# Performance work log

Hardware: AMD Instinct MI355X
Metric: run time of the kernel (lower is better)

Reference implementation:

```python
import jax, jax.numpy as jnp
import numpy as np

B, T, E, H = 8, 1024, 1024, 16
D = E // H  # head_dim = 64
MAX_OFFSET = 0.5


def setup_inputs() -> dict:
    key = jax.random.key(0)
    ks = jax.random.split(key, 12)
    s = 0.02
    return {
        "query": jax.random.normal(ks[0], (B, T, E), jnp.float32),
        "key_": jax.random.normal(ks[1], (B, T, E), jnp.float32),
        "value": jax.random.normal(ks[2], (B, T, E), jnp.float32),
        "Wq": jax.random.normal(ks[3], (E, E), jnp.float32) * s,
        "bq": jnp.zeros((E,), jnp.float32),
        "Wk": jax.random.normal(ks[4], (E, E), jnp.float32) * s,
        "bk": jnp.zeros((E,), jnp.float32),
        "Wv": jax.random.normal(ks[5], (E, E), jnp.float32) * s,
        "bv": jnp.zeros((E,), jnp.float32),
        "Wo": jax.random.normal(ks[6], (E, E), jnp.float32) * s,
        "bo": jnp.zeros((E,), jnp.float32),
        "bias_table": jax.random.normal(ks[7], (2 * T - 1, H), jnp.float32) * s,
        "offset": jax.random.normal(ks[8], (1,), jnp.float32) * 0.1,
    }


def _temporal_bias(bias_table, offset):
    # relative position index: [T, T] in [0, 2T-2]
    coords = jnp.arange(T)
    rel = (coords[:, None] - coords[None, :]) + (T - 1)
    bounded = jnp.tanh(offset) * MAX_OFFSET  # scalar (shape (1,))
    adj = jnp.clip(rel.astype(jnp.float32) + bounded, 0.0, 2.0 * T - 2.0)
    lo = jnp.floor(adj).astype(jnp.int32)
    hi = jnp.ceil(adj).astype(jnp.int32)
    w = adj - lo.astype(jnp.float32)  # [T, T]
    lo_val = bias_table[lo]  # [T, T, H]
    hi_val = bias_table[hi]  # [T, T, H]
    bias = lo_val * (1.0 - w[..., None]) + hi_val * w[..., None]
    # -> [1, H, T, T]
    return jnp.transpose(bias, (2, 0, 1))[None]


def reference(query, key_, value, Wq, bq, Wk, bk, Wv, bv, Wo, bo, bias_table, offset):
    scale = D ** -0.5
    # torch Linear: x @ W.T + b
    q = (jnp.einsum('bte,fe->btf', query, Wq) + bq).reshape(B, T, H, D).transpose(0, 2, 1, 3)
    k = (jnp.einsum('bte,fe->btf', key_, Wk) + bk).reshape(B, T, H, D).transpose(0, 2, 1, 3)
    v = (jnp.einsum('bte,fe->btf', value, Wv) + bv).reshape(B, T, H, D).transpose(0, 2, 1, 3)
    scores = jnp.einsum('bhqd,bhkd->bhqk', q, k) * scale  # [B, H, T, T]
    scores = scores + _temporal_bias(bias_table, offset)
    attn = jax.nn.softmax(scores, axis=-1)
    out = jnp.einsum('bhqk,bhkd->bhqd', attn, v)  # [B, H, T, D]
    out = out.transpose(0, 2, 1, 3).reshape(B, T, E)
    return jnp.einsum('bte,fe->btf', out, Wo) + bo
```

## Files before the change

### kernel.cpp

```cpp
#include <hip/hip_runtime.h>
#include <hip/hip_bf16.h>
#include <stdint.h>

#define B_ 8
#define T_ 1024
#define E_ 1024
#define H_ 16
#define D_ 64
#define NREL 2047

using bf16 = __hip_bfloat16;
typedef __attribute__((ext_vector_type(8))) short bhalf8;
typedef __attribute__((ext_vector_type(4))) float f32x4;

typedef __attribute__((address_space(3))) uint32_t lds32_t;
typedef const __attribute__((address_space(1))) uint32_t glb32_t;
__device__ __forceinline__ void gld_lds16(const bf16* g, bf16* l) {
  __builtin_amdgcn_global_load_lds((glb32_t*)(const void*)g, (lds32_t*)(void*)l, 16, 0, 0);
}

__device__ __forceinline__ bhalf8 cvt8(const float4 a, const float4 b) {
  bf16 t[8];
  t[0] = __float2bfloat16(a.x); t[1] = __float2bfloat16(a.y);
  t[2] = __float2bfloat16(a.z); t[3] = __float2bfloat16(a.w);
  t[4] = __float2bfloat16(b.x); t[5] = __float2bfloat16(b.y);
  t[6] = __float2bfloat16(b.z); t[7] = __float2bfloat16(b.w);
  return *(const bhalf8*)t;
}

__global__ __launch_bounds__(256) void cvt_w4b(const float* __restrict__ Wq,
                                               const float* __restrict__ Wk,
                                               const float* __restrict__ Wv,
                                               const float* __restrict__ Wo,
                                               bf16* __restrict__ d,
                                               const float* __restrict__ table,
                                               const float* __restrict__ offset,
                                               float* __restrict__ db) {
  const int z = blockIdx.y;
  if (z == 4) {
    const int idx = blockIdx.x * 256 + threadIdx.x;
    if (idx >= NREL * H_) return;
    const int r = idx >> 4;
    const int h = idx & 15;
    const float bounded = tanhf(offset[0]) * 0.5f;
    float adj = (float)r + bounded;
    adj = fminf(fmaxf(adj, 0.f), 2046.f);
    const int lo = (int)floorf(adj);
    const int hi = (int)ceilf(adj);
    const float wgt = adj - (float)lo;
    const float v = table[lo * H_ + h] * (1.f - wgt) + table[hi * H_ + h] * wgt;
    db[h * NREL + r] = v * 1.4426950408889634f;
    return;
  }
  const float* s = (z == 0) ? Wq : (z == 1) ? Wk : (z == 2) ? Wv : Wo;
  const int i = (blockIdx.x * 256 + threadIdx.x) * 8;
  const float4 a = *(const float4*)(s + i);
  const float4 b = *(const float4*)(s + i + 4);
  *(bhalf8*)(d + (size_t)z * E_ * E_ + i) = cvt8(a, b);
}

__global__ __launch_bounds__(256, 3) void gemm_qkv(const float* __restrict__ Xq,
                                                   const float* __restrict__ Xk,
                                                   const float* __restrict__ Xv,
                                                   const bf16* __restrict__ Wc,
                                                   const float* __restrict__ bqp,
                                                   const float* __restrict__ bkp,
                                                   const float* __restrict__ bvp,
                                                   bf16* __restrict__ dst) {
  __shared__ bf16 As[2 * 128 * 32];
  __shared__ bf16 Bs[3 * 128 * 32];
  const int tid = threadIdx.x;
  const int lane = tid & 63;
  const int w = tid >> 6;
  const int quad = lane >> 4;
  const int l15 = lane & 15;
  const int m0 = blockIdx.x * 128;
  const int n0 = blockIdx.y * 128;
  const int z = blockIdx.z;
  const float* A = (z == 0) ? Xq : ((z == 1) ? Xk : Xv);
  const float* bias = (z == 0) ? bqp : ((z == 1) ? bkp : bvp);
  const bf16* W = Wc + (size_t)z * E_ * E_;
  bf16* out = dst + (size_t)z * B_ * T_ * D_ * H_;
  const int wm = (w >> 1) * 64;
  const int wn = (w & 1) * 64;

  const f32x4 zero4 = {0.f, 0.f, 0.f, 0.f};
  f32x4 acc[4][4];
#pragma unroll
  for (int i = 0; i < 4; ++i)
#pragma unroll
    for (int j = 0; j < 4; ++j) acc[i][j] = zero4;

  const int srow = w * 32 + (lane >> 2);
  const int scol = (lane & 3) * 8;
  const float* Ag = A + (size_t)(m0 + srow) * E_ + scol;
  const bf16* Wg = W + (size_t)(n0 + srow) * E_ + scol;
  const int sidx = w * 1024 + lane * 8;

  {
    float4 a0 = *(const float4*)(Ag);
    float4 a1 = *(const float4*)(Ag + 4);
    float4 a2 = *(const float4*)(Ag + (size_t)16 * E_);
    float4 a3 = *(const float4*)(Ag + (size_t)16 * E_ + 4);
    *(bhalf8*)(As + sidx) = cvt8(a0, a1);
    *(bhalf8*)(As + sidx + 512) = cvt8(a2, a3);
  }
  gld_lds16(Wg, Bs + sidx);
  gld_lds16(Wg + (size_t)16 * E_, Bs + sidx + 512);
  gld_lds16(Wg + 32, Bs + 4096 + sidx);
  gld_lds16(Wg + (size_t)16 * E_ + 32, Bs + 4096 + sidx + 512);
  float4 p0 = *(const float4*)(Ag + 32);
  float4 p1 = *(const float4*)(Ag + 36);
  float4 p2 = *(const float4*)(Ag + (size_t)16 * E_ + 32);
  float4 p3 = *(const float4*)(Ag + (size_t)16 * E_ + 36);
  asm volatile("s_waitcnt vmcnt(6)" ::: "memory");
  asm volatile("s_waitcnt lgkmcnt(0)" ::: "memory");
  __builtin_amdgcn_s_barrier();
  __builtin_amdgcn_sched_barrier(0);

  int cB = 0;
  int cB2 = 2;
  for (int kt = 0; kt < 32; ++kt) {
    const int curA = (kt & 1) * 4096;
    bhalf8 af[4], bfr[4];
#pragma unroll
    for (int t2 = 0; t2 < 4; ++t2) {
      af[t2] = *(const bhalf8*)(As + curA + (wm + t2 * 16 + l15) * 32 + quad * 8);
      bfr[t2] = *(const bhalf8*)(Bs + cB * 4096 + (wn + t2 * 16 + l15) * 32 + quad * 8);
    }
    if (kt < 30) {
      const int kcW = (kt + 2) * 32;
      gld_lds16(Wg + kcW, Bs + cB2 * 4096 + sidx);
      gld_lds16(Wg + (size_t)16 * E_ + kcW, Bs + cB2 * 4096 + sidx + 512);
    }
    if (kt < 31) {
      const int nxtA = 4096 - curA;
      *(bhalf8*)(As + nxtA + sidx) = cvt8(p0, p1);
      *(bhalf8*)(As + nxtA + sidx + 512) = cvt8(p2, p3);
      if (kt < 30) {
        const int kc2 = (kt + 2) * 32;
        p0 = *(const float4*)(Ag + kc2);
        p1 = *(const float4*)(Ag + kc2 + 4);
        p2 = *(const float4*)(Ag + (size_t)16 * E_ + kc2);
        p3 = *(const float4*)(Ag + (size_t)16 * E_ + kc2 + 4);
      }
    }
#pragma unroll
    for (int mt = 0; mt < 4; ++mt)
#pragma unroll
      for (int nt = 0; nt < 4; ++nt)
        acc[mt][nt] = __builtin_amdgcn_mfma_f32_16x16x32_bf16(af[mt], bfr[nt], acc[mt][nt], 0, 0, 0);
    if (kt < 30) {
      asm volatile("s_waitcnt vmcnt(6)" ::: "memory");
      asm volatile("s_waitcnt lgkmcnt(0)" ::: "memory");
    } else {
      asm volatile("s_waitcnt vmcnt(0) lgkmcnt(0)" ::: "memory");
    }
    __builtin_amdgcn_s_barrier();
    __builtin_amdgcn_sched_barrier(0);
    cB = (cB == 2) ? 0 : cB + 1;
    cB2 = (cB2 == 2) ? 0 : cB2 + 1;
  }

#pragma unroll
  for (int mt = 0; mt < 4; ++mt) {
#pragma unroll
    for (int nt = 0; nt < 4; ++nt) {
      const int n = n0 + wn + nt * 16 + l15;
      const float bv = bias[n];
#pragma unroll
      for (int r = 0; r < 4; ++r) {
        const int m = m0 + wm + mt * 16 + quad * 4 + r;
        const float v = acc[mt][nt][r] + bv;
        const int bb = m >> 10, tq = m & 1023, hh = n >> 6, d = n & 63;
        out[(((size_t)bb * H_ + hh) * T_ + tq) * D_ + d] = __float2bfloat16(v);
      }
    }
  }
}

template <int SCATTER, int F32OUT>
__global__ __launch_bounds__(256, 4) void gemm_bt(const bf16* __restrict__ A,
                                                  const bf16* __restrict__ W,
                                                  const float* __restrict__ bias,
                                                  void* __restrict__ dst_) {
  __shared__ bf16 As[2 * 64 * 32];
  __shared__ bf16 Bs[2 * 128 * 32];
  const int tid = threadIdx.x;
  const int lane = tid & 63;
  const int w = tid >> 6;
  const int quad = lane >> 4;
  const int l15 = lane & 15;
  const int m0 = blockIdx.x * 64;
  const int n0 = blockIdx.y * 128;
  const int wm = (w >> 1) * 32;
  const int wn = (w & 1) * 64;

  const f32x4 zero4 = {0.f, 0.f, 0.f, 0.f};
  f32x4 acc[2][4];
#pragma unroll
  for (int i = 0; i < 2; ++i)
#pragma unroll
    for (int j = 0; j < 4; ++j) acc[i][j] = zero4;

  const int scol = (lane & 3) * 8;
  const int srowA = w * 16 + (lane >> 2);
  const bf16* Ag = A + (size_t)(m0 + srowA) * E_ + scol;
  const int sidxA = w * 512 + lane * 8;
  const int srowB = w * 32 + (lane >> 2);
  const bf16* Wg = W + (size_t)(n0 + srowB) * E_ + scol;
  const int sidxB = w * 1024 + lane * 8;

  gld_lds16(Ag, As + sidxA);
  gld_lds16(Wg, Bs + sidxB);
  gld_lds16(Wg + (size_t)16 * E_, Bs + sidxB + 512);
  __syncthreads();

  for (int kt = 0; kt < 32; ++kt) {
    const int curA = (kt & 1) * 2048;
    const int curB = (kt & 1) * 4096;
    bhalf8 af[2], bfr[4];
#pragma unroll
    for (int mt = 0; mt < 2; ++mt)
      af[mt] = *(const bhalf8*)(As + curA + (wm + mt * 16 + l15) * 32 + quad * 8);
#pragma unroll
    for (int nt = 0; nt < 4; ++nt)
      bfr[nt] = *(const bhalf8*)(Bs + curB + (wn + nt * 16 + l15) * 32 + quad * 8);
    if (kt < 31) {
      const int nxtA = 2048 - curA;
      const int nxtB = 4096 - curB;
      const int kc = (kt + 1) * 32;
      gld_lds16(Ag + kc, As + nxtA + sidxA);
      gld_lds16(Wg + kc, Bs + nxtB + sidxB);
      gld_lds16(Wg + (size_t)16 * E_ + kc, Bs + nxtB + sidxB + 512);
    }
#pragma unroll
    for (int mt = 0; mt < 2; ++mt)
#pragma unroll
      for (int nt = 0; nt < 4; ++nt)
        acc[mt][nt] = __builtin_amdgcn_mfma_f32_16x16x32_bf16(af[mt], bfr[nt], acc[mt][nt], 0, 0, 0);
    __syncthreads();
  }

#pragma unroll
  for (int mt = 0; mt < 2; ++mt) {
#pragma unroll
    for (int nt = 0; nt < 4; ++nt) {
      const int n = n0 + wn + nt * 16 + l15;
      const float bv = bias[n];
#pragma unroll
      for (int r = 0; r < 4; ++r) {
        const int m = m0 + wm + mt * 16 + quad * 4 + r;
        const float v = acc[mt][nt][r] + bv;
        if (SCATTER) {
          const int bb = m >> 10, t = m & 1023, hh = n >> 6, d = n & 63;
          ((bf16*)dst_)[(((size_t)bb * H_ + hh) * T_ + t) * D_ + d] = __float2bfloat16(v);
        } else if (F32OUT) {
          ((float*)dst_)[(size_t)m * E_ + n] = v;
        } else {
          ((bf16*)dst_)[(size_t)m * E_ + n] = __float2bfloat16(v);
        }
      }
    }
  }
}

__device__ __forceinline__ int ps_off(int row, int colbyte) {
  return row * 128 + (colbyte ^ ((row & 7) << 4));
}

__global__ __launch_bounds__(256, 4) void attn_kernel(const bf16* __restrict__ Q,
                                                      const bf16* __restrict__ K,
                                                      const bf16* __restrict__ V,
                                                      const float* __restrict__ db,
                                                      bf16* __restrict__ xout) {
  const int tid = threadIdx.x;
  const int lane = tid & 63;
  const int w = tid >> 6;
  const int quad = lane >> 4;
  const int l15 = lane & 15;
  const int bh = blockIdx.x;
  const int h = bh & 15;
  const int b = bh >> 4;
  const int q0 = blockIdx.y * 128;

  __shared__ bf16 Vt[64][72];
  __shared__ __align__(16) bf16 Ps[4][32 * 64];
  __shared__ float dbs[1152];

  const size_t base = (size_t)bh * T_ * D_;
  const bf16* Qp = Q + base;
  const bf16* Kp = K + base;
  const bf16* Vp = V + base;
  const float* dbh = db + h * NREL;

  for (int t = tid; t < 1151; t += 256) dbs[t] = dbh[q0 + t];

  const int qw = q0 + w * 32;
  bhalf8 aq[2][2];
#pragma unroll
  for (int mt = 0; mt < 2; ++mt)
#pragma unroll
    for (int ks = 0; ks < 2; ++ks)
      aq[mt][ks] = *(const bhalf8*)(Qp + (size_t)(qw + mt * 16 + l15) * D_ + ks * 32 + quad * 8);

  const f32x4 zero4 = {0.f, 0.f, 0.f, 0.f};
  f32x4 o[2][4];
#pragma unroll
  for (int mt = 0; mt < 2; ++mt)
#pragma unroll
    for (int nt = 0; nt < 4; ++nt) o[mt][nt] = zero4;
  float mrow[2] = {-1e30f, -1e30f};
  float lrow[2] = {0.f, 0.f};

  const int vrow0 = tid >> 3;
  const int vc8 = (tid & 7) * 8;
  bhalf8 vreg[2];
  vreg[0] = *(const bhalf8*)(Vp + (size_t)vrow0 * D_ + vc8);
  vreg[1] = *(const bhalf8*)(Vp + (size_t)(vrow0 + 32) * D_ + vc8);

  char* const psw = (char*)&Ps[w][0];

  for (int it = 0; it < 16; ++it) {
    const int kb = it * 64;
    bhalf8 bk[4][2];
#pragma unroll
    for (int nt = 0; nt < 4; ++nt) {
      const bf16* kr = Kp + (size_t)(kb + nt * 16 + l15) * D_ + quad * 8;
      bk[nt][0] = *(const bhalf8*)kr;
      bk[nt][1] = *(const bhalf8*)(kr + 32);
    }

    __syncthreads();
#pragma unroll
    for (int s = 0; s < 2; ++s) {
      const int row = vrow0 + s * 32;
      const bf16* vp = (const bf16*)&vreg[s];
      const int kvp = (row + vc8) & 63;
#pragma unroll
      for (int j = 0; j < 8; ++j) Vt[vc8 + j][kvp] = vp[j];
    }
    __syncthreads();
    if (it < 15) {
      const int kb2 = kb + 64;
      vreg[0] = *(const bhalf8*)(Vp + (size_t)(kb2 + vrow0) * D_ + vc8);
      vreg[1] = *(const bhalf8*)(Vp + (size_t)(kb2 + vrow0 + 32) * D_ + vc8);
    }

    f32x4 s4[2][4];
    __builtin_amdgcn_s_setprio(1);
#pragma unroll
    for (int nt = 0; nt < 4; ++nt) {
#pragma unroll
      for (int mt = 0; mt < 2; ++mt) {
        f32x4 a = zero4;
        a = __builtin_amdgcn_mfma_f32_16x16x32_bf16(bk[nt][0], aq[mt][0], a, 0, 0, 0);
        a = __builtin_amdgcn_mfma_f32_16x16x32_bf16(bk[nt][1], aq[mt][1], a, 0, 0, 0);
        s4[mt][nt] = a;
      }
    }
    __builtin_amdgcn_s_setprio(0);

#pragma unroll
    for (int mt = 0; mt < 2; ++mt) {
      const int ib = w * 32 + mt * 16 + l15 + 1023 - kb;
      float mnt[4];
#pragma unroll
      for (int nt = 0; nt < 4; ++nt) {
#pragma unroll
        for (int r = 0; r < 4; ++r) {
          const float sv = s4[mt][nt][r] * 0.18033688011112042f + dbs[ib - nt * 16 - quad * 4 - r];
          s4[mt][nt][r] = sv;
        }
        mnt[nt] = fmaxf(fmaxf(s4[mt][nt][0], s4[mt][nt][1]),
                        fmaxf(s4[mt][nt][2], s4[mt][nt][3]));
      }
      float tmx = fmaxf(fmaxf(mnt[0], mnt[1]), fmaxf(mnt[2], mnt[3]));
      tmx = fmaxf(tmx, __shfl_xor(tmx, 16, 64));
      tmx = fmaxf(tmx, __shfl_xor(tmx, 32, 64));
      if (!__all(tmx - mrow[mt] <= 11.0f)) {
        const float mnew = fmaxf(mrow[mt], tmx);
        const float alpha = __builtin_amdgcn_exp2f(mrow[mt] - mnew);
        mrow[mt] = mnew;
        lrow[mt] *= alpha;
#pragma unroll
        for (int nt = 0; nt < 4; ++nt) o[mt][nt] *= alpha;
      }
      const float mcur = mrow[mt];
      float psum[4];
#pragma unroll
      for (int nt = 0; nt < 4; ++nt) {
        float p0 = __builtin_amdgcn_exp2f(s4[mt][nt][0] - mcur);
        float p1 = __builtin_amdgcn_exp2f(s4[mt][nt][1] - mcur);
        float p2 = __builtin_amdgcn_exp2f(s4[mt][nt][2] - mcur);
        float p3 = __builtin_amdgcn_exp2f(s4[mt][nt][3] - mcur);
        s4[mt][nt][0] = p0; s4[mt][nt][1] = p1;
        s4[mt][nt][2] = p2; s4[mt][nt][3] = p3;
        psum[nt] = (p0 + p1) + (p2 + p3);
      }
      float sum = (psum[0] + psum[1]) + (psum[2] + psum[3]);
      sum += __shfl_xor(sum, 16, 64);
      sum += __shfl_xor(sum, 32, 64);
      lrow[mt] += sum;

#pragma unroll
      for (int nt = 0; nt < 4; ++nt) {
        alignas(8) bf16 t4[4];
#pragma unroll
        for (int r = 0; r < 4; ++r) t4[r] = __float2bfloat16(s4[mt][nt][r]);
        *(uint2*)(psw + ps_off(mt * 16 + l15, nt * 32 + quad * 8)) = *(const uint2*)t4;
      }
    }

    bhalf8 pb[2][2];
#pragma unroll
    for (int mt = 0; mt < 2; ++mt)
#pragma unroll
      for (int ks = 0; ks < 2; ++ks)
        pb[mt][ks] = *(const bhalf8*)(psw + ps_off(mt * 16 + l15, ks * 64 + quad * 16));
    const int rot = (l15 >> 3);
    __builtin_amdgcn_s_setprio(1);
#pragma unroll
    for (int nt = 0; nt < 4; ++nt) {
      const int drow = nt * 16 + l15;
#pragma unroll
      for (int ks = 0; ks < 2; ++ks) {
        const int gp = (4 * ks + quad + 2 * nt + rot) & 7;
        const bhalf8 vb = *(const bhalf8*)&Vt[drow][gp * 8];
#pragma unroll
        for (int mt = 0; mt < 2; ++mt)
          o[mt][nt] = __builtin_amdgcn_mfma_f32_16x16x32_bf16(vb, pb[mt][ks], o[mt][nt], 0, 0, 0);
      }
    }
    __builtin_amdgcn_s_setprio(0);
  }

#pragma unroll
  for (int mt = 0; mt < 2; ++mt) {
    const float inv = 1.f / lrow[mt];
#pragma unroll
    for (int nt = 0; nt < 4; ++nt) {
      alignas(8) bf16 t4[4];
#pragma unroll
      for (int r = 0; r < 4; ++r) t4[r] = __float2bfloat16(o[mt][nt][r] * inv);
      *(uint2*)(psw + ps_off(mt * 16 + l15, nt * 32 + quad * 8)) = *(const uint2*)t4;
    }
  }
#pragma unroll
  for (int t = 0; t < 4; ++t) {
    const int idx = t * 64 + lane;
    const int row = idx >> 3;
    const int c = idx & 7;
    const bhalf8 val = *(const bhalf8*)(psw + ps_off(row, c * 16));
    *(bhalf8*)&xout[((size_t)b * T_ + qw + row) * E_ + h * D_ + c * 8] = val;
  }
}

extern "C" void kernel_launch(void* const* d_in, const int* in_sizes, int n_in,
                              void* d_out, int out_size, void* d_ws, size_t ws_size,
                              hipStream_t stream) {
  const float* query = (const float*)d_in[0];
  const float* key_  = (const float*)d_in[1];
  const float* value = (const float*)d_in[2];
  const float* Wq = (const float*)d_in[3];
  const float* bq = (const float*)d_in[4];
  const float* Wk = (const float*)d_in[5];
  const float* bk = (const float*)d_in[6];
  const float* Wv = (const float*)d_in[7];
  const float* bv = (const float*)d_in[8];
  const float* Wo = (const float*)d_in[9];
  const float* bo = (const float*)d_in[10];
  const float* table = (const float*)d_in[11];
  const float* offset = (const float*)d_in[12];
  float* out = (float*)d_out;

  char* ws = (char*)d_ws;
  const size_t ME = (size_t)B_ * T_ * E_;
  const size_t EE = (size_t)E_ * E_;
  float* db = (float*)ws;
  bf16* wc  = (bf16*)(ws + 131072);
  bf16* qb  = wc + 4 * EE;
  bf16* kb  = qb + ME;
  bf16* vb2 = kb + ME;
  bf16* x2  = vb2 + ME;

  dim3 bb(256, 1, 1);
  const int gEE = (int)(EE / 8 / 256);

  cvt_w4b<<<dim3(gEE, 5), bb, 0, stream>>>(Wq, Wk, Wv, Wo, wc, table, offset, db);

  gemm_qkv<<<dim3(64, 8, 3), bb, 0, stream>>>(query, key_, value, wc, bq, bk, bv, qb);

  attn_kernel<<<dim3(128, 8, 1), bb, 0, stream>>>(qb, kb, vb2, db, x2);

  gemm_bt<0, 1><<<dim3(128, 8, 1), bb, 0, stream>>>(x2, wc + 3 * EE, bo, out);
}
```

Baseline: 350.6 us.

## Stage fp32 activations into LDS via direct global loads, convert at fragment read

The QKV projection GEMM now loads fp32 activation tiles straight into LDS with global_load_lds, using an XOR-swizzled layout. Each fragment read converts them to bf16, replacing the old register-prefetch-and-convert staging. The weight buffer goes from a 3-stage to a 2-stage ring, and the manual vmcnt waits are replaced by a plain __syncthreads per k-step. This frees registers and simplifies the pipeline, but the fp32 A tile doubles its LDS footprint and reads. The conversion is now redone by every wave that reads a fragment, and the shallower pipeline may expose more load latency.

```diff
diff --git a/kernel.cpp b/kernel.cpp
--- a/kernel.cpp
+++ b/kernel.cpp
@@ -15,8 +15,8 @@
 
 typedef __attribute__((address_space(3))) uint32_t lds32_t;
 typedef const __attribute__((address_space(1))) uint32_t glb32_t;
-__device__ __forceinline__ void gld_lds16(const bf16* g, bf16* l) {
-  __builtin_amdgcn_global_load_lds((glb32_t*)(const void*)g, (lds32_t*)(void*)l, 16, 0, 0);
+__device__ __forceinline__ void gld_lds16(const void* g, void* l) {
+  __builtin_amdgcn_global_load_lds((glb32_t*)g, (lds32_t*)l, 16, 0, 0);
 }
 
 __device__ __forceinline__ bhalf8 cvt8(const float4 a, const float4 b) {
@@ -67,8 +67,8 @@
                                                    const float* __restrict__ bkp,
                                                    const float* __restrict__ bvp,
                                                    bf16* __restrict__ dst) {
-  __shared__ bf16 As[2 * 128 * 32];
-  __shared__ bf16 Bs[3 * 128 * 32];
+  __shared__ float AsF[2 * 128 * 32];
+  __shared__ bf16 Bs[2 * 128 * 32];
   const int tid = threadIdx.x;
   const int lane = tid & 63;
   const int w = tid >> 6;
@@ -91,75 +91,55 @@
 #pragma unroll
     for (int j = 0; j < 4; ++j) acc[i][j] = zero4;
 
-  const int srow = w * 32 + (lane >> 2);
-  const int scol = (lane & 3) * 8;
-  const float* Ag = A + (size_t)(m0 + srow) * E_ + scol;
-  const bf16* Wg = W + (size_t)(n0 + srow) * E_ + scol;
-  const int sidx = w * 1024 + lane * 8;
-
-  {
-    float4 a0 = *(const float4*)(Ag);
-    float4 a1 = *(const float4*)(Ag + 4);
-    float4 a2 = *(const float4*)(Ag + (size_t)16 * E_);
-    float4 a3 = *(const float4*)(Ag + (size_t)16 * E_ + 4);
-    *(bhalf8*)(As + sidx) = cvt8(a0, a1);
-    *(bhalf8*)(As + sidx + 512) = cvt8(a2, a3);
-  }
-  gld_lds16(Wg, Bs + sidx);
-  gld_lds16(Wg + (size_t)16 * E_, Bs + sidx + 512);
-  gld_lds16(Wg + 32, Bs + 4096 + sidx);
-  gld_lds16(Wg + (size_t)16 * E_ + 32, Bs + 4096 + sidx + 512);
-  float4 p0 = *(const float4*)(Ag + 32);
-  float4 p1 = *(const float4*)(Ag + 36);
-  float4 p2 = *(const float4*)(Ag + (size_t)16 * E_ + 32);
-  float4 p3 = *(const float4*)(Ag + (size_t)16 * E_ + 36);
-  asm volatile("s_waitcnt vmcnt(6)" ::: "memory");
-  asm volatile("s_waitcnt lgkmcnt(0)" ::: "memory");
-  __builtin_amdgcn_s_barrier();
-  __builtin_amdgcn_sched_barrier(0);
-
-  int cB = 0;
-  int cB2 = 2;
+  const int g = tid;
+  const int arow = g >> 3;
+  const int acol = (((g & 7) ^ ((g >> 3) & 7)) << 2);
+  const float* Ag = A + (size_t)(m0 + arow) * E_ + acol;
+  float* AsDst = AsF + g * 4;
+  const int srowW = w * 32 + (lane >> 2);
+  const int scolW = (lane & 3) * 8;
+  const bf16* Wg = W + (size_t)(n0 + srowW) * E_ + scolW;
+  bf16* BsDst = Bs + w * 1024 + lane * 8;
+
+#pragma unroll
+  for (int c = 0; c < 4; ++c)
+    gld_lds16(Ag + (size_t)c * 32 * E_, AsDst + c * 1024);
+  gld_lds16(Wg, BsDst);
+  gld_lds16(Wg + (size_t)16 * E_, BsDst + 512);
+  __syncthreads();
+
   for (int kt = 0; kt < 32; ++kt) {
     const int curA = (kt & 1) * 4096;
+    const int curB = (kt & 1) * 4096;
     bhalf8 af[4], bfr[4];
 #pragma unroll
-    for (int t2 = 0; t2 < 4; ++t2) {
-      af[t2] = *(const bhalf8*)(As + curA + (wm + t2 * 16 + l15) * 32 + quad * 8);
-      bfr[t2] = *(const bhalf8*)(Bs + cB * 4096 + (wn + t2 * 16 + l15) * 32 + quad * 8);
-    }
-    if (kt < 30) {
-      const int kcW = (kt + 2) * 32;
-      gld_lds16(Wg + kcW, Bs + cB2 * 4096 + sidx);
-      gld_lds16(Wg + (size_t)16 * E_ + kcW, Bs + cB2 * 4096 + sidx + 512);
-    }
+    for (int mt = 0; mt < 4; ++mt) {
+      const int row = wm + mt * 16 + l15;
+      const int cb = (quad * 32) ^ ((row & 7) << 4);
+      const char* rp = (const char*)(AsF + curA + row * 32);
+      const float4 lo = *(const float4*)(rp + cb);
+      const float4 hi = *(const float4*)(rp + (cb ^ 16));
+      af[mt] = cvt8(lo, hi);
+    }
+#pragma unroll
+    for (int nt = 0; nt < 4; ++nt)
+      bfr[nt] = *(const bhalf8*)(Bs + curB + (wn + nt * 16 + l15) * 32 + quad * 8);
     if (kt < 31) {
       const int nxtA = 4096 - curA;
-      *(bhalf8*)(As + nxtA + sidx) = cvt8(p0, p1);
-      *(bhalf8*)(As + nxtA + sidx + 512) = cvt8(p2, p3);
-      if (kt < 30) {
-        const int kc2 = (kt + 2) * 32;
-        p0 = *(const float4*)(Ag + kc2);
-        p1 = *(const float4*)(Ag + kc2 + 4);
-        p2 = *(const float4*)(Ag + (size_t)16 * E_ + kc2);
-        p3 = *(const float4*)(Ag + (size_t)16 * E_ + kc2 + 4);
-      }
+      const int nxtB = 4096 - curB;
+      const int kc = (kt + 1) * 32;
+#pragma unroll
+      for (int c = 0; c < 4; ++c)
+        gld_lds16(Ag + (size_t)c * 32 * E_ + kc, AsDst + nxtA + c * 1024);
+      gld_lds16(Wg + kc, BsDst + nxtB);
+      gld_lds16(Wg + (size_t)16 * E_ + kc, BsDst + nxtB + 512);
     }
 #pragma unroll
     for (int mt = 0; mt < 4; ++mt)
 #pragma unroll
       for (int nt = 0; nt < 4; ++nt)
         acc[mt][nt] = __builtin_amdgcn_mfma_f32_16x16x32_bf16(af[mt], bfr[nt], acc[mt][nt], 0, 0, 0);
-    if (kt < 30) {
-      asm volatile("s_waitcnt vmcnt(6)" ::: "memory");
-      asm volatile("s_waitcnt lgkmcnt(0)" ::: "memory");
-    } else {
-      asm volatile("s_waitcnt vmcnt(0) lgkmcnt(0)" ::: "memory");
-    }
-    __builtin_amdgcn_s_barrier();
-    __builtin_amdgcn_sched_barrier(0);
-    cB = (cB == 2) ? 0 : cB + 1;
-    cB2 = (cB2 == 2) ? 0 : cB2 + 1;
+    __syncthreads();
   }
 
 #pragma unroll
```

New measurement: 352.2 us. About the same (+0.5%).
